# Optimization experiments

Measured on AMD Instinct MI355X. Metric: run time of the kernel, lower is better.

## Reference

```python
import jax, jax.numpy as jnp
import numpy as np

N = 100000   # nodes
M = 200000   # gathered (combined-subgraph) node entries
E = 600000   # combined-subgraph edges
B = 128      # graphs
P = 32       # patches per graph (METIS)
BP = B * P
DIN = 64; H = 256; RW = 16
L = 4        # GCN layers
LM = 4       # mixer layers
T = 64       # token-mixing hidden dim
CH = 4 * H   # channel-mixing hidden dim
DOUT = 10


def _seg_mean(v, idx, n):
    s = jax.ops.segment_sum(v, idx, num_segments=n)
    c = jax.ops.segment_sum(jnp.ones((v.shape[0],), v.dtype), idx, num_segments=n)
    return s / jnp.maximum(c, 1.0)[:, None]


def _ln(x, s, b):
    m = jnp.mean(x, -1, keepdims=True)
    v = jnp.var(x, -1, keepdims=True)
    return (x - m) * jax.lax.rsqrt(v + 1e-5) * s + b


def setup_inputs() -> dict:
    key = jax.random.key(0)
    ks = jax.random.split(key, 40)
    w = lambda k, s: jax.random.normal(k, s, jnp.float32) * 0.02
    inp = {
        'x': jax.random.normal(ks[0], (N, DIN), jnp.float32),
        'patch_pe': jax.random.normal(ks[1], (BP, RW), jnp.float32),
        'mask': jnp.ones((B, P), jnp.bool_),
        'nodes_mapper': jax.random.randint(ks[2], (M,), 0, N),
        'subgraphs_batch': jnp.sort(jax.random.randint(ks[3], (M,), 0, BP)),
        'edge_index': jax.random.randint(ks[4], (2, E), 0, M),
        # pre_mp
        'W_pre': w(ks[5], (DIN, H)), 'b_pre': jnp.zeros((H,), jnp.float32),
        # U MLPs (layers-1 of them) and GCN weights
        'W_u': w(ks[6], (L - 1, H, H)), 'b_u': jnp.zeros((L - 1, H), jnp.float32),
        'W_g': w(ks[7], (L, H, H)), 'b_g': jnp.zeros((L, H), jnp.float32),
        # patch RW-PE 2-layer MLP
        'Wp1': w(ks[8], (RW, H)), 'bp1': jnp.zeros((H,), jnp.float32),
        'Wp2': w(ks[9], (H, H)), 'bp2': jnp.zeros((H,), jnp.float32),
        # MLPMixer blocks (stacked over LM layers)
        'ln1_s': jnp.ones((LM, H), jnp.float32), 'ln1_b': jnp.zeros((LM, H), jnp.float32),
        'Wt1': w(ks[10], (LM, P, T)), 'bt1': jnp.zeros((LM, T), jnp.float32),
        'Wt2': w(ks[11], (LM, T, P)), 'bt2': jnp.zeros((LM, P), jnp.float32),
        'ln2_s': jnp.ones((LM, H), jnp.float32), 'ln2_b': jnp.zeros((LM, H), jnp.float32),
        'Wc1': w(ks[12], (LM, H, CH)), 'bc1': jnp.zeros((LM, CH), jnp.float32),
        'Wc2': w(ks[13], (LM, CH, H)), 'bc2': jnp.zeros((LM, H), jnp.float32),
        # head
        'ln_f_s': jnp.ones((H,), jnp.float32), 'ln_f_b': jnp.zeros((H,), jnp.float32),
        'W_head': w(ks[14], (H, DOUT)), 'b_head': jnp.zeros((DOUT,), jnp.float32),
    }
    return inp


def reference(x, patch_pe, mask, nodes_mapper, subgraphs_batch, edge_index,
              W_pre, b_pre, W_u, b_u, W_g, b_g, Wp1, bp1, Wp2, bp2,
              ln1_s, ln1_b, Wt1, bt1, Wt2, bt2, ln2_s, ln2_b, Wc1, bc1, Wc2, bc2,
              ln_f_s, ln_f_b, W_head, b_head):
    # pre_mp: linear + relu on node features [N, H]
    h = jax.nn.relu(x @ W_pre + b_pre)
    # gather nodes into combined-subgraph space [M, H]
    h = h[nodes_mapper]
    src, dst = edge_index[0], edge_index[1]
    # GCN symmetric normalization with self loops (degree over M-space)
    deg = jax.ops.segment_sum(jnp.ones((src.shape[0],), h.dtype), dst, num_segments=M) + 1.0
    nrm = jax.lax.rsqrt(deg)
    edge_nrm = (nrm[src] * nrm[dst])[:, None]
    self_nrm = (nrm * nrm)[:, None]
    for i in range(L):
        if i > 0:
            # pre_layer_scatter: pool per subgraph, broadcast back, add U-MLP
            sub = _seg_mean(h, subgraphs_batch, BP)[subgraphs_batch]
            h = h + jax.nn.relu(sub @ W_u[i - 1] + b_u[i - 1])
            # post_layer_scatter: mean over duplicated nodes, broadcast back
            h = _seg_mean(h, nodes_mapper, N)[nodes_mapper]
        # GCNConv + relu
        hw = h @ W_g[i]
        agg = jax.ops.segment_sum(hw[src] * edge_nrm, dst, num_segments=M)
        h = jax.nn.relu(agg + hw * self_nrm + b_g[i])
    # final_scatter: pool to [B*P, H]
    h = _seg_mean(h, subgraphs_batch, BP)
    # patch random-walk PE encoder (2-layer MLP) added
    pe = jax.nn.relu(jax.nn.relu(patch_pe @ Wp1 + bp1) @ Wp2 + bp2)
    z = (h + pe).reshape(B, P, H)
    # MLPMixer
    for l in range(LM):
        y = jnp.swapaxes(_ln(z, ln1_s[l], ln1_b[l]), 1, 2)  # [B, H, P]
        y = jax.nn.gelu(y @ Wt1[l] + bt1[l]) @ Wt2[l] + bt2[l]
        z = z + jnp.swapaxes(y, 1, 2)
        y = _ln(z, ln2_s[l], ln2_b[l])
        z = z + (jax.nn.gelu(y @ Wc1[l] + bc1[l]) @ Wc2[l] + bc2[l])
    # masked mean pooling over patches
    m = mask.astype(z.dtype)
    g = (z * m[:, :, None]).sum(1) / m.sum(1, keepdims=True)
    # head
    g = _ln(g, ln_f_s, ln_f_b)
    return g @ W_head + b_head
```

## Files before the change

kernel.cpp:

```cpp
#include <hip/hip_runtime.h>
#include <math.h>

namespace {

typedef unsigned short u16;
typedef unsigned int u32;
typedef unsigned long long u64;
typedef __attribute__((ext_vector_type(8))) short bf16x8;
typedef __attribute__((ext_vector_type(8))) unsigned short u16x8;
typedef __attribute__((ext_vector_type(4))) float f32x4;

constexpr int kN = 100000, kM = 200000, kE = 600000;
constexpr int kB = 128, kP = 32, kBP = kB * kP;
constexpr int kDIN = 64, kH = 256, kRW = 16;
constexpr int kL = 4, kLM = 4, kT = 64, kCH = 4 * kH, kDOUT = 10;
constexpr int kScanCB = 1024;

__device__ __forceinline__ float geluf(float x) {
  const float c = 0.7978845608028654f;
  float x3 = x * x * x;
  return 0.5f * x * (1.f + tanhf(c * (x + 0.044715f * x3)));
}

__device__ __forceinline__ float bf2f(u16 h) {
  u32 u = ((u32)h) << 16;
  return __uint_as_float(u);
}
__device__ __forceinline__ u16 f2bf(float f) {
  u32 u = __float_as_uint(f);
  u32 r = (u + 0x7FFFu + ((u >> 16) & 1u)) >> 16;
  return (u16)r;
}
__device__ __forceinline__ float4 bf4_to_f4(ushort4 v) {
  return make_float4(bf2f(v.x), bf2f(v.y), bf2f(v.z), bf2f(v.w));
}
__device__ __forceinline__ ushort4 f4_to_bf4(float4 v) {
  ushort4 r;
  r.x = f2bf(v.x); r.y = f2bf(v.y); r.z = f2bf(v.z); r.w = f2bf(v.w);
  return r;
}

template <int RPT>
__global__ __launch_bounds__(256) void k_gemm(
    const float* __restrict__ A, const float* __restrict__ B,
    const float* __restrict__ bias, const float* __restrict__ res,
    float* __restrict__ C, int Mr, int Nc, int Kc, int act) {
  constexpr int BM = 16 * RPT;
  __shared__ float As[16][BM];
  __shared__ float Bs[16][64];
  int tid = threadIdx.x;
  int tx = tid & 15, ty = tid >> 4;
  int bm = blockIdx.x * BM, bn = blockIdx.y * 64;
  float acc[RPT][4];
#pragma unroll
  for (int i = 0; i < RPT; ++i)
#pragma unroll
    for (int j = 0; j < 4; ++j) acc[i][j] = 0.f;

  for (int k0 = 0; k0 < Kc; k0 += 16) {
#pragma unroll
    for (int l = 0; l < RPT / 4; ++l) {
      int idx = tid + l * 256;
      int r = idx >> 2, c4 = (idx & 3) * 4;
      float4 a4 = make_float4(0.f, 0.f, 0.f, 0.f);
      if (bm + r < Mr) a4 = *(const float4*)(A + (size_t)(bm + r) * Kc + k0 + c4);
      As[c4 + 0][r] = a4.x; As[c4 + 1][r] = a4.y;
      As[c4 + 2][r] = a4.z; As[c4 + 3][r] = a4.w;
    }
    {
      int kr = tid >> 4, cc = (tid & 15) * 4;
      float4 b4 = *(const float4*)(B + (size_t)(k0 + kr) * Nc + bn + cc);
      *(float4*)&Bs[kr][cc] = b4;
    }
    __syncthreads();
#pragma unroll
    for (int k = 0; k < 16; ++k) {
      float a[RPT], bb[4];
#pragma unroll
      for (int l = 0; l < RPT / 4; ++l) {
        float4 av = *(const float4*)&As[k][ty * RPT + l * 4];
        a[l * 4 + 0] = av.x; a[l * 4 + 1] = av.y;
        a[l * 4 + 2] = av.z; a[l * 4 + 3] = av.w;
      }
      float4 bv = *(const float4*)&Bs[k][tx * 4];
      bb[0] = bv.x; bb[1] = bv.y; bb[2] = bv.z; bb[3] = bv.w;
#pragma unroll
      for (int i = 0; i < RPT; ++i)
#pragma unroll
        for (int j = 0; j < 4; ++j) acc[i][j] = fmaf(a[i], bb[j], acc[i][j]);
    }
    __syncthreads();
  }
#pragma unroll
  for (int i = 0; i < RPT; ++i) {
    int row = bm + ty * RPT + i;
    if (row >= Mr) continue;
#pragma unroll
    for (int j = 0; j < 4; ++j) {
      int col = bn + tx * 4 + j;
      float v = acc[i][j];
      if (bias) v += bias[col];
      if (act == 1) v = fmaxf(v, 0.f);
      else if (act == 2) v = geluf(v);
      if (res) v += res[(size_t)row * Nc + col];
      C[(size_t)row * Nc + col] = v;
    }
  }
}

__global__ void k_packw(const float* __restrict__ W, u16* __restrict__ Wp,
                        int KB, int NC, int L) {
  int per = KB * NC * 16 * 64;
  int o8 = blockIdx.x * 256 + threadIdx.x;
  if (o8 >= L * per) return;
  int li = o8 / per, r = o8 % per;
  int l = r & 63;
  int t = r >> 6;
  int nt = t & 15, q = t >> 4;
  int kbg = q % KB, nc = q / KB;
  int Kc = KB * 32, Ncols = NC * 256;
  int col = nc * 256 + nt * 16 + (l & 15);
  int k0 = kbg * 32 + (l >> 4) * 8;
  const float* w = W + (size_t)li * Kc * Ncols;
  u16* o = Wp + (size_t)o8 * 8;
#pragma unroll
  for (int i = 0; i < 8; ++i) o[i] = f2bf(w[(size_t)(k0 + i) * Ncols + col]);
}

__global__ __launch_bounds__(256) void k_gemm_rowblk_mfma(
    const u16* A, const u16* __restrict__ Wp, u16* C, int Mr) {
  __shared__ u16 As[64 * 256];
  __shared__ u16 Bs[8192];
  int tid = threadIdx.x;
  int w = tid >> 6, l = tid & 63;
  int bm = blockIdx.x * 64;
  u16x8 pre[4];
#pragma unroll
  for (int j = 0; j < 4; ++j) pre[j] = *(const u16x8*)(Wp + tid * 8 + j * 2048);
#pragma unroll
  for (int i = 0; i < 8; ++i) {
    int idx = tid + i * 256;
    int row = idx >> 5, seg = idx & 31;
    u16x8 v = (u16x8){0, 0, 0, 0, 0, 0, 0, 0};
    if (bm + row < Mr) v = *(const u16x8*)(A + (size_t)(bm + row) * 256 + seg * 8);
    *(u16x8*)((char*)As + row * 512 + ((seg * 16) ^ ((row & 15) << 4))) = v;
  }

  f32x4 acc[16];
#pragma unroll
  for (int nt = 0; nt < 16; ++nt) acc[nt] = (f32x4){0.f, 0.f, 0.f, 0.f};
  int a_row = w * 16 + (l & 15);
  int a_xor = (a_row & 15) << 4;
  for (int kb = 0; kb < 8; ++kb) {
    __syncthreads();
#pragma unroll
    for (int j = 0; j < 4; ++j) *(u16x8*)(Bs + tid * 8 + j * 2048) = pre[j];
    __syncthreads();
    if (kb < 7) {
#pragma unroll
      for (int j = 0; j < 4; ++j)
        pre[j] = *(const u16x8*)(Wp + (kb + 1) * 8192 + tid * 8 + j * 2048);
    }
    int abyte = a_row * 512 + ((kb * 64 + (l >> 4) * 16) ^ a_xor);
    bf16x8 af = *(const bf16x8*)((const char*)As + abyte);
#pragma unroll
    for (int nt = 0; nt < 16; ++nt) {
      bf16x8 bf = *(const bf16x8*)(Bs + nt * 512 + l * 8);
      acc[nt] = __builtin_amdgcn_mfma_f32_16x16x32_bf16(af, bf, acc[nt], 0, 0, 0);
    }
  }
  __syncthreads();
  int c_row0 = w * 16 + (l >> 4) * 4;
  int ccol = l & 15;
#pragma unroll
  for (int nt = 0; nt < 16; ++nt) {
#pragma unroll
    for (int j = 0; j < 4; ++j) {
      int row = c_row0 + j;
      int colbyte = (nt * 16 + ccol) * 2;
      *(u16*)((char*)As + row * 512 + (colbyte ^ ((row & 15) << 4))) = f2bf(acc[nt][j]);
    }
  }
  __syncthreads();
#pragma unroll
  for (int i = 0; i < 8; ++i) {
    int idx = tid + i * 256;
    int row = idx >> 5, seg = idx & 31;
    if (bm + row < Mr) {
      u16x8 v = *(const u16x8*)((const char*)As + row * 512 + ((seg * 16) ^ ((row & 15) << 4)));
      *(u16x8*)(C + (size_t)(bm + row) * 256 + seg * 8) = v;
    }
  }
}

__global__ __launch_bounds__(256) void k_gemm_mfma_s(
    const void* __restrict__ Av, const u16* __restrict__ Wp,
    const float* __restrict__ bias, const float* __restrict__ res,
    void* __restrict__ Cv, int Kc, int Ncols, int act, int outw, int abf) {
  __shared__ u16 As[64 * 256];
  __shared__ u16 Bs[8192];
  int tid = threadIdx.x;
  int w = tid >> 6, l = tid & 63;
  int bm = blockIdx.x * 64;
  int nchunk = blockIdx.y, bn = nchunk * 256;
  int KB = Kc >> 5;
  const u16* wseq = Wp + (size_t)nchunk * KB * 8192;

  u16x8 pre[4];
#pragma unroll
  for (int j = 0; j < 4; ++j) pre[j] = *(const u16x8*)(wseq + tid * 8 + j * 2048);

  f32x4 acc[16];
#pragma unroll
  for (int nt = 0; nt < 16; ++nt) acc[nt] = (f32x4){0.f, 0.f, 0.f, 0.f};
  int a_row = w * 16 + (l & 15);
  int a_xor = (a_row & 15) << 4;

  for (int kc0 = 0; kc0 < Kc; kc0 += 256) {
    __syncthreads();
#pragma unroll
    for (int i = 0; i < 8; ++i) {
      int idx = tid + i * 256;
      int row = idx >> 5, seg = idx & 31;
      u16x8 hv;
      if (abf) {
        hv = *(const u16x8*)((const u16*)Av + (size_t)(bm + row) * Kc + kc0 + seg * 8);
      } else {
        const float* s = (const float*)Av + (size_t)(bm + row) * Kc + kc0 + seg * 8;
        float4 v0 = *(const float4*)s;
        float4 v1 = *(const float4*)(s + 4);
        hv[0] = f2bf(v0.x); hv[1] = f2bf(v0.y); hv[2] = f2bf(v0.z); hv[3] = f2bf(v0.w);
        hv[4] = f2bf(v1.x); hv[5] = f2bf(v1.y); hv[6] = f2bf(v1.z); hv[7] = f2bf(v1.w);
      }
      *(u16x8*)((char*)As + row * 512 + ((seg * 16) ^ ((row & 15) << 4))) = hv;
    }
    int kbg0 = kc0 >> 5;
    for (int kb = 0; kb < 8; ++kb) {
      int t = kbg0 + kb;
      __syncthreads();
#pragma unroll
      for (int j = 0; j < 4; ++j) *(u16x8*)(Bs + tid * 8 + j * 2048) = pre[j];
      __syncthreads();
      if (t + 1 < KB) {
#pragma unroll
        for (int j = 0; j < 4; ++j)
          pre[j] = *(const u16x8*)(wseq + (size_t)(t + 1) * 8192 + tid * 8 + j * 2048);
      }
      int abyte = a_row * 512 + ((kb * 64 + (l >> 4) * 16) ^ a_xor);
      bf16x8 af = *(const bf16x8*)((const char*)As + abyte);
#pragma unroll
      for (int nt = 0; nt < 16; ++nt) {
        bf16x8 bf = *(const bf16x8*)(Bs + nt * 512 + l * 8);
        acc[nt] = __builtin_amdgcn_mfma_f32_16x16x32_bf16(af, bf, acc[nt], 0, 0, 0);
      }
    }
  }

  int c_row0 = w * 16 + (l >> 4) * 4;
  int ccol = l & 15;
  if (outw == 1) {
    float* C = (float*)Cv;
#pragma unroll
    for (int nt = 0; nt < 16; ++nt) {
      int col = bn + nt * 16 + ccol;
      float bv = bias[col];
#pragma unroll
      for (int j = 0; j < 4; ++j) {
        int row = bm + c_row0 + j;
        float v = acc[nt][j] + bv;
        if (act == 1) v = fmaxf(v, 0.f);
        else if (act == 2) v = geluf(v);
        if (res) v += res[(size_t)row * Ncols + col];
        C[(size_t)row * Ncols + col] = v;
      }
    }
  } else {
    u16* C = (u16*)Cv;
    __syncthreads();
#pragma unroll
    for (int nt = 0; nt < 16; ++nt) {
      float bv = bias[bn + nt * 16 + ccol];
#pragma unroll
      for (int j = 0; j < 4; ++j) {
        int row = c_row0 + j;
        float v = acc[nt][j] + bv;
        if (act == 1) v = fmaxf(v, 0.f);
        else if (act == 2) v = geluf(v);
        int colbyte = (nt * 16 + ccol) * 2;
        *(u16*)((char*)As + row * 512 + (colbyte ^ ((row & 15) << 4))) = f2bf(v);
      }
    }
    __syncthreads();
#pragma unroll
    for (int i = 0; i < 8; ++i) {
      int idx = tid + i * 256;
      int row = idx >> 5, seg = idx & 31;
      u16x8 v = *(const u16x8*)((const char*)As + row * 512 + ((seg * 16) ^ ((row & 15) << 4)));
      *(u16x8*)(C + (size_t)(bm + row) * Ncols + bn + seg * 8) = v;
    }
  }
}

__global__ __launch_bounds__(256) void k_premp_mfma(
    const float* __restrict__ A, const u16* __restrict__ Wp,
    const float* __restrict__ bias, u16* __restrict__ C, int Mr) {
  __shared__ u16 As[64 * 256];
  __shared__ u16 Bs[8192];
  int tid = threadIdx.x;
  int w = tid >> 6, l = tid & 63;
  int bm = blockIdx.x * 64;
  u16x8 pre[4];
#pragma unroll
  for (int j = 0; j < 4; ++j) pre[j] = *(const u16x8*)(Wp + tid * 8 + j * 2048);
#pragma unroll
  for (int i = 0; i < 2; ++i) {
    int idx = tid + i * 256;
    int row = idx >> 3, seg = idx & 7;
    u16x8 hv = (u16x8){0, 0, 0, 0, 0, 0, 0, 0};
    if (bm + row < Mr) {
      const float* s = A + (size_t)(bm + row) * 64 + seg * 8;
      float4 v0 = *(const float4*)s;
      float4 v1 = *(const float4*)(s + 4);
      hv[0] = f2bf(v0.x); hv[1] = f2bf(v0.y); hv[2] = f2bf(v0.z); hv[3] = f2bf(v0.w);
      hv[4] = f2bf(v1.x); hv[5] = f2bf(v1.y); hv[6] = f2bf(v1.z); hv[7] = f2bf(v1.w);
    }
    *(u16x8*)((char*)As + row * 128 + ((seg * 16) ^ ((row & 7) << 4))) = hv;
  }

  f32x4 acc[16];
#pragma unroll
  for (int nt = 0; nt < 16; ++nt) acc[nt] = (f32x4){0.f, 0.f, 0.f, 0.f};
  int a_row = w * 16 + (l & 15);
#pragma unroll
  for (int kb = 0; kb < 2; ++kb) {
    __syncthreads();
#pragma unroll
    for (int j = 0; j < 4; ++j) *(u16x8*)(Bs + tid * 8 + j * 2048) = pre[j];
    __syncthreads();
    if (kb == 0) {
#pragma unroll
      for (int j = 0; j < 4; ++j)
        pre[j] = *(const u16x8*)(Wp + 8192 + tid * 8 + j * 2048);
    }
    int abyte = a_row * 128 + ((kb * 64 + (l >> 4) * 16) ^ ((a_row & 7) << 4));
    bf16x8 af = *(const bf16x8*)((const char*)As + abyte);
#pragma unroll
    for (int nt = 0; nt < 16; ++nt) {
      bf16x8 bf = *(const bf16x8*)(Bs + nt * 512 + l * 8);
      acc[nt] = __builtin_amdgcn_mfma_f32_16x16x32_bf16(af, bf, acc[nt], 0, 0, 0);
    }
  }
  __syncthreads();
  int c_row0 = w * 16 + (l >> 4) * 4;
  int ccol = l & 15;
#pragma unroll
  for (int nt = 0; nt < 16; ++nt) {
    float bv = bias[nt * 16 + ccol];
#pragma unroll
    for (int j = 0; j < 4; ++j) {
      int row = c_row0 + j;
      float v = fmaxf(acc[nt][j] + bv, 0.f);
      int colbyte = (nt * 16 + ccol) * 2;
      *(u16*)((char*)As + row * 512 + (colbyte ^ ((row & 15) << 4))) = f2bf(v);
    }
  }
  __syncthreads();
#pragma unroll
  for (int i = 0; i < 8; ++i) {
    int idx = tid + i * 256;
    int row = idx >> 5, seg = idx & 31;
    if (bm + row < Mr) {
      u16x8 v = *(const u16x8*)((const char*)As + row * 512 + ((seg * 16) ^ ((row & 15) << 4)));
      *(u16x8*)(C + (size_t)(bm + row) * 256 + seg * 8) = v;
    }
  }
}

__global__ void k_hist(const int* __restrict__ idx, int* __restrict__ cnt, int n) {
  int i = blockIdx.x * 256 + threadIdx.x;
  if (i < n) atomicAdd(&cnt[idx[i]], 1);
}

__global__ __launch_bounds__(256) void k_scan_a(const int* __restrict__ cnt, int n,
                                                int* __restrict__ bsum) {
  __shared__ int red[256];
  int b = blockIdx.x, t = threadIdx.x;
  int base = b * kScanCB + t * 4;
  int s = 0;
#pragma unroll
  for (int j = 0; j < 4; ++j) { int i = base + j; if (i < n) s += cnt[i]; }
  red[t] = s;
  __syncthreads();
  for (int d = 128; d; d >>= 1) {
    if (t < d) red[t] += red[t + d];
    __syncthreads();
  }
  if (t == 0) bsum[b] = red[0];
}

__global__ __launch_bounds__(256) void k_scan_b(const int* __restrict__ bsum, int G,
                                                int* __restrict__ boff,
                                                int* __restrict__ total_out) {
  __shared__ int sd[256];
  int t = threadIdx.x;
  sd[t] = (t < G) ? bsum[t] : 0;
  __syncthreads();
  for (int d = 1; d < 256; d <<= 1) {
    int u = (t >= d) ? sd[t - d] : 0;
    __syncthreads();
    sd[t] += u;
    __syncthreads();
  }
  if (t < G) boff[t] = t ? sd[t - 1] : 0;
  if (t == 255) *total_out = sd[255];
}

__global__ __launch_bounds__(256) void k_scan_c(const int* __restrict__ cnt, int n,
                                                const int* __restrict__ boff,
                                                int* __restrict__ out) {
  __shared__ int sd[256];
  int b = blockIdx.x, t = threadIdx.x;
  int base = b * kScanCB + t * 4;
  int c[4];
  int s = 0;
#pragma unroll
  for (int j = 0; j < 4; ++j) {
    int i = base + j;
    c[j] = (i < n) ? cnt[i] : 0;
    s += c[j];
  }
  sd[t] = s;
  __syncthreads();
  for (int d = 1; d < 256; d <<= 1) {
    int u = (t >= d) ? sd[t - d] : 0;
    __syncthreads();
    sd[t] += u;
    __syncthreads();
  }
  int run = boff[b] + (t ? sd[t - 1] : 0);
#pragma unroll
  for (int j = 0; j < 4; ++j) {
    int i = base + j;
    if (i < n) out[i] = run;
    run += c[j];
  }
}

__global__ void k_nrm(const int* __restrict__ cnt, float* __restrict__ nrm, int n) {
  int i = blockIdx.x * 256 + threadIdx.x;
  if (i < n) nrm[i] = rsqrtf((float)cnt[i] + 1.f);
}

__global__ void k_scatter_e(const int* __restrict__ src, const int* __restrict__ dst,
                            const int* __restrict__ nmap, const float* __restrict__ nrm,
                            const int* __restrict__ rs, int* __restrict__ cur,
                            int* __restrict__ gidx, float* __restrict__ w) {
  int e = blockIdx.x * 256 + threadIdx.x;
  if (e >= kE) return;
  int s = src[e], d = dst[e];
  int p = rs[d] + atomicAdd(&cur[d], 1);
  gidx[p] = nmap[s];
  w[p] = nrm[s] * nrm[d];
}

__global__ void k_scatter_m(const int* __restrict__ nmap, const int* __restrict__ rs,
                            int* __restrict__ cur, int* __restrict__ lst) {
  int m = blockIdx.x * 256 + threadIdx.x;
  if (m >= kM) return;
  int n = nmap[m];
  int p = rs[n] + atomicAdd(&cur[n], 1);
  lst[p] = m;
}

__global__ void k_bpstart(const int* __restrict__ sb, int* __restrict__ bps) {
  int bp = blockIdx.x * 256 + threadIdx.x;
  if (bp > kBP) return;
  if (bp == kBP) { bps[kBP] = kM; return; }
  int lo = 0, hi = kM;
  while (lo < hi) { int mid = (lo + hi) >> 1; if (sb[mid] < bp) lo = mid + 1; else hi = mid; }
  bps[bp] = lo;
}

__global__ __launch_bounds__(256) void k_pool_seg_b(const u16* __restrict__ h,
                                                    const int* __restrict__ bps,
                                                    float* __restrict__ out) {
  int bp = blockIdx.x, j = threadIdx.x;
  int lo = bps[bp], hi = bps[bp + 1];
  float s = 0.f;
  for (int m = lo; m < hi; ++m) s += bf2f(h[(size_t)m * kH + j]);
  out[(size_t)bp * kH + j] = s / fmaxf((float)(hi - lo), 1.f);
}

__global__ __launch_bounds__(256) void k_pool_n_f(const u16* __restrict__ h,
                                                  const float* __restrict__ ub,
                                                  const int* __restrict__ sb,
                                                  const int* __restrict__ rs,
                                                  const int* __restrict__ lst,
                                                  u16* __restrict__ outp) {
  int wv = threadIdx.x >> 6, lane = threadIdx.x & 63;
  int n = blockIdx.x * 4 + wv;
  if (n >= kN) return;
  int lo = rs[n], hi = rs[n + 1];
  float4 acc = make_float4(0.f, 0.f, 0.f, 0.f);
  for (int p = lo; p < hi; ++p) {
    int m = lst[p];
    union { u64 u; ushort4 s; } cv;
    cv.u = __builtin_nontemporal_load((const u64*)(h + (size_t)m * 256 + lane * 4));
    float4 v = bf4_to_f4(cv.s);
    float4 u = ((const float4*)ub)[(size_t)sb[m] * 64 + lane];
    acc.x += v.x + u.x; acc.y += v.y + u.y;
    acc.z += v.z + u.z; acc.w += v.w + u.w;
  }
  float inv = 1.f / fmaxf((float)(hi - lo), 1.f);
  acc.x *= inv; acc.y *= inv; acc.z *= inv; acc.w *= inv;
  *(ushort4*)(outp + (size_t)n * 256 + lane * 4) = f4_to_bf4(acc);
}

__global__ __launch_bounds__(256) void k_gcn_b(const u16* __restrict__ hw,
                                               const int* __restrict__ nmap,
                                               const float* __restrict__ nrm,
                                               const int* __restrict__ rs,
                                               const int* __restrict__ gidx,
                                               const float* __restrict__ w,
                                               const float* __restrict__ bias,
                                               u16* __restrict__ outp) {
  int wv = threadIdx.x >> 6, lane = threadIdx.x & 63;
  int m = blockIdx.x * 4 + wv;
  if (m >= kM) return;
  float nm_ = nrm[m];
  float sn = nm_ * nm_;
  float4 b4 = ((const float4*)bias)[lane];
  float4 sv = bf4_to_f4(*(const ushort4*)(hw + (size_t)nmap[m] * 256 + lane * 4));
  float4 acc;
  acc.x = fmaf(sv.x, sn, b4.x); acc.y = fmaf(sv.y, sn, b4.y);
  acc.z = fmaf(sv.z, sn, b4.z); acc.w = fmaf(sv.w, sn, b4.w);
  int lo = rs[m], hi = rs[m + 1];
  for (int p0 = lo; p0 < hi; p0 += 4) {
    int last = hi - 1;
    int q1 = min(p0 + 1, last), q2 = min(p0 + 2, last), q3 = min(p0 + 3, last);
    int g0 = gidx[p0], g1 = gidx[q1], g2 = gidx[q2], g3 = gidx[q3];
    float w0 = w[p0];
    float w1 = (p0 + 1 < hi) ? w[q1] : 0.f;
    float w2 = (p0 + 2 < hi) ? w[q2] : 0.f;
    float w3 = (p0 + 3 < hi) ? w[q3] : 0.f;
    float4 v0 = bf4_to_f4(*(const ushort4*)(hw + (size_t)g0 * 256 + lane * 4));
    float4 v1 = bf4_to_f4(*(const ushort4*)(hw + (size_t)g1 * 256 + lane * 4));
    float4 v2 = bf4_to_f4(*(const ushort4*)(hw + (size_t)g2 * 256 + lane * 4));
    float4 v3 = bf4_to_f4(*(const ushort4*)(hw + (size_t)g3 * 256 + lane * 4));
    acc.x = fmaf(v3.x, w3, fmaf(v2.x, w2, fmaf(v1.x, w1, fmaf(v0.x, w0, acc.x))));
    acc.y = fmaf(v3.y, w3, fmaf(v2.y, w2, fmaf(v1.y, w1, fmaf(v0.y, w0, acc.y))));
    acc.z = fmaf(v3.z, w3, fmaf(v2.z, w2, fmaf(v1.z, w1, fmaf(v0.z, w0, acc.z))));
    acc.w = fmaf(v3.w, w3, fmaf(v2.w, w2, fmaf(v1.w, w1, fmaf(v0.w, w0, acc.w))));
  }
  acc.x = fmaxf(acc.x, 0.f); acc.y = fmaxf(acc.y, 0.f);
  acc.z = fmaxf(acc.z, 0.f); acc.w = fmaxf(acc.w, 0.f);
  *(ushort4*)(outp + (size_t)m * 256 + lane * 4) = f4_to_bf4(acc);
}

__global__ __launch_bounds__(256) void k_ln(const float* __restrict__ x,
                                            const float* __restrict__ s,
                                            const float* __restrict__ b,
                                            float* __restrict__ y) {
  __shared__ float t1[4], t2[4];
  int r = blockIdx.x, j = threadIdx.x;
  float v = x[(size_t)r * kH + j];
  float a = v, q = v * v;
  for (int o = 32; o; o >>= 1) { a += __shfl_down(a, o, 64); q += __shfl_down(q, o, 64); }
  if ((j & 63) == 0) { t1[j >> 6] = a; t2[j >> 6] = q; }
  __syncthreads();
  float sum = t1[0] + t1[1] + t1[2] + t1[3];
  float sq = t2[0] + t2[1] + t2[2] + t2[3];
  float mu = sum * (1.f / 256.f);
  float var = sq * (1.f / 256.f) - mu * mu;
  y[(size_t)r * kH + j] = (v - mu) * rsqrtf(var + 1e-5f) * s[j] + b[j];
}

__global__ __launch_bounds__(256) void k_token(const float* __restrict__ zn,
                                               const float* __restrict__ Wt1,
                                               const float* __restrict__ bt1,
                                               const float* __restrict__ Wt2,
                                               const float* __restrict__ bt2,
                                               float* __restrict__ z) {
  __shared__ float zs[32][65];
  __shared__ float w1[32][64];
  __shared__ float w2[64][33];
  __shared__ float y1[64][65];
  int bb = blockIdx.x, hb = blockIdx.y * 64;
  int t = threadIdx.x;
  for (int i = t; i < 2048; i += 256) {
    int p = i >> 6, hh = i & 63;
    zs[p][hh] = zn[((size_t)bb * 32 + p) * kH + hb + hh];
  }
  for (int i = t; i < 2048; i += 256) { int p = i >> 6, tt = i & 63; w1[p][tt] = Wt1[p * 64 + tt]; }
  for (int i = t; i < 2048; i += 256) { int tt = i >> 5, p = i & 31; w2[tt][p] = Wt2[tt * 32 + p]; }
  __syncthreads();
  for (int i = t; i < 4096; i += 256) {
    int hh = i >> 6, tt = i & 63;
    float a = bt1[tt];
#pragma unroll
    for (int p = 0; p < 32; ++p) a = fmaf(zs[p][hh], w1[p][tt], a);
    y1[hh][tt] = geluf(a);
  }
  __syncthreads();
  for (int i = t; i < 2048; i += 256) {
    int hh = i >> 5, p = i & 31;
    float a = bt2[p];
#pragma unroll
    for (int tt = 0; tt < 64; ++tt) a = fmaf(y1[hh][tt], w2[tt][p], a);
    z[((size_t)bb * 32 + p) * kH + hb + hh] += a;
  }
}

__global__ void k_gpool(const float* __restrict__ z, float* __restrict__ g) {
  int bb = blockIdx.x, j = threadIdx.x;
  float s = 0.f;
  for (int p = 0; p < 32; ++p) s += z[((size_t)bb * 32 + p) * kH + j];
  g[bb * kH + j] = s * (1.f / 32.f);
}

__global__ __launch_bounds__(256) void k_head(const float* __restrict__ g,
                                              const float* __restrict__ s,
                                              const float* __restrict__ b,
                                              const float* __restrict__ Wh,
                                              const float* __restrict__ bh,
                                              float* __restrict__ out) {
  __shared__ float t1[4], t2[4];
  __shared__ float row[256];
  int bb = blockIdx.x, j = threadIdx.x;
  float v = g[bb * kH + j];
  float a = v, q = v * v;
  for (int o = 32; o; o >>= 1) { a += __shfl_down(a, o, 64); q += __shfl_down(q, o, 64); }
  if ((j & 63) == 0) { t1[j >> 6] = a; t2[j >> 6] = q; }
  __syncthreads();
  float sum = t1[0] + t1[1] + t1[2] + t1[3];
  float sq = t2[0] + t2[1] + t2[2] + t2[3];
  float mu = sum * (1.f / 256.f);
  float var = sq * (1.f / 256.f) - mu * mu;
  row[j] = (v - mu) * rsqrtf(var + 1e-5f) * s[j] + b[j];
  __syncthreads();
  if (j < kDOUT) {
    float acc = bh[j];
    for (int k = 0; k < kH; ++k) acc = fmaf(row[k], Wh[k * kDOUT + j], acc);
    out[bb * kDOUT + j] = acc;
  }
}

}

extern "C" void kernel_launch(void* const* d_in, const int* in_sizes, int n_in,
                              void* d_out, int out_size, void* d_ws, size_t ws_size,
                              hipStream_t stream) {
  const float* x = (const float*)d_in[0];
  const float* ppe = (const float*)d_in[1];
  const int* nmap = (const int*)d_in[3];
  const int* sb = (const int*)d_in[4];
  const int* esrc = (const int*)d_in[5];
  const int* edst = esrc + kE;
  const float* Wpre = (const float*)d_in[6];
  const float* bpre = (const float*)d_in[7];
  const float* Wu = (const float*)d_in[8];
  const float* bu = (const float*)d_in[9];
  const float* Wg = (const float*)d_in[10];
  const float* bg = (const float*)d_in[11];
  const float* Wp1 = (const float*)d_in[12];
  const float* bp1 = (const float*)d_in[13];
  const float* Wp2 = (const float*)d_in[14];
  const float* bp2 = (const float*)d_in[15];
  const float* ln1s = (const float*)d_in[16];
  const float* ln1b = (const float*)d_in[17];
  const float* Wt1 = (const float*)d_in[18];
  const float* bt1 = (const float*)d_in[19];
  const float* Wt2 = (const float*)d_in[20];
  const float* bt2 = (const float*)d_in[21];
  const float* ln2s = (const float*)d_in[22];
  const float* ln2b = (const float*)d_in[23];
  const float* Wc1 = (const float*)d_in[24];
  const float* bc1 = (const float*)d_in[25];
  const float* Wc2 = (const float*)d_in[26];
  const float* bc2 = (const float*)d_in[27];
  const float* lnfs = (const float*)d_in[28];
  const float* lnfb = (const float*)d_in[29];
  const float* Whd = (const float*)d_in[30];
  const float* bhd = (const float*)d_in[31];
  float* out = (float*)d_out;

  u16* h_M = (u16*)d_ws;
  u16* h_N = h_M + (size_t)kM * kH;
  float* sub = (float*)(h_N + (size_t)kN * kH);
  float* ubuf = sub + (size_t)kBP * kH;
  float* csrw = ubuf + (size_t)kBP * kH;
  float* nrm = csrw + kE;
  int* rsE = (int*)(nrm + kM);
  int* gidx = rsE + kM + 1;
  int* rsN = gidx + kE;
  int* mlst = rsN + kN + 1;
  int* cntE = mlst + kM;
  int* cntN = cntE + kM;
  int* bps = cntN + kN;
  int* bsumS = bps + kBP + 1;
  int* boffS = bsumS + 256;
  size_t need = ((size_t)(boffS + 256)) - ((size_t)d_ws);
  if (ws_size < need) {
    hipMemsetAsync(d_out, 0, (size_t)out_size * sizeof(float), stream);
    return;
  }

  u16* wpackG = (u16*)(((size_t)cntE + 15) & ~(size_t)15);
  u16* wpackPre = wpackG + 4 * 65536;
  u16* wpackU = wpackPre + 16384;

  float* z = (float*)d_ws;
  float* zn = z + (size_t)kBP * kH;
  float* c1 = zn + (size_t)kBP * kH;
  float* g = c1 + (size_t)kBP * kCH;
  u16* wpackC = (u16*)(g + kB * kH);
  u16* wpackC2 = wpackC + 4 * 262144;
  u16* wpackP2 = wpackC2 + 4 * 262144;

  hipMemsetAsync(cntE, 0, kM * sizeof(int), stream);
  hipMemsetAsync(cntN, 0, kN * sizeof(int), stream);

  constexpr int GscanM = (kM + kScanCB - 1) / kScanCB;
  constexpr int GscanN = (kN + kScanCB - 1) / kScanCB;

  k_hist<<<(kE + 255) / 256, 256, 0, stream>>>(edst, cntE, kE);
  k_hist<<<(kM + 255) / 256, 256, 0, stream>>>(nmap, cntN, kM);
  k_scan_a<<<GscanM, 256, 0, stream>>>(cntE, kM, bsumS);
  k_scan_b<<<1, 256, 0, stream>>>(bsumS, GscanM, boffS, rsE + kM);
  k_scan_c<<<GscanM, 256, 0, stream>>>(cntE, kM, boffS, rsE);
  k_scan_a<<<GscanN, 256, 0, stream>>>(cntN, kN, bsumS);
  k_scan_b<<<1, 256, 0, stream>>>(bsumS, GscanN, boffS, rsN + kN);
  k_scan_c<<<GscanN, 256, 0, stream>>>(cntN, kN, boffS, rsN);
  k_nrm<<<(kM + 255) / 256, 256, 0, stream>>>(cntE, nrm, kM);
  hipMemsetAsync(cntE, 0, kM * sizeof(int), stream);
  hipMemsetAsync(cntN, 0, kN * sizeof(int), stream);
  k_scatter_e<<<(kE + 255) / 256, 256, 0, stream>>>(esrc, edst, nmap, nrm, rsE, cntE, gidx, csrw);
  k_scatter_m<<<(kM + 255) / 256, 256, 0, stream>>>(nmap, rsN, cntN, mlst);
  k_bpstart<<<(kBP + 256) / 256, 256, 0, stream>>>(sb, bps);
  k_packw<<<(4 * 8192 + 255) / 256, 256, 0, stream>>>(Wg, wpackG, 8, 1, 4);
  k_packw<<<(2048 + 255) / 256, 256, 0, stream>>>(Wpre, wpackPre, 2, 1, 1);
  k_packw<<<(3 * 8192 + 255) / 256, 256, 0, stream>>>(Wu, wpackU, 8, 1, 3);

  k_premp_mfma<<<(kN + 63) / 64, 256, 0, stream>>>(x, wpackPre, bpre, h_N, kN);

  for (int i = 0; i < kL; ++i) {
    if (i > 0) {
      k_pool_seg_b<<<kBP, 256, 0, stream>>>(h_M, bps, sub);
      k_gemm_mfma_s<<<dim3(64, 1), 256, 0, stream>>>(
          sub, wpackU + (size_t)(i - 1) * 65536, bu + (i - 1) * kH, nullptr,
          ubuf, 256, 256, 1, 1, 0);
      k_pool_n_f<<<(kN + 3) / 4, 256, 0, stream>>>(h_M, ubuf, sb, rsN, mlst, h_N);
    }
    k_gemm_rowblk_mfma<<<(kN + 63) / 64, 256, 0, stream>>>(
        h_N, wpackG + (size_t)i * 65536, h_N, kN);
    k_gcn_b<<<(kM + 3) / 4, 256, 0, stream>>>(h_N, nmap, nrm, rsE, gidx, csrw, bg + i * kH, h_M);
  }

  k_pool_seg_b<<<kBP, 256, 0, stream>>>(h_M, bps, sub);
  k_packw<<<(4 * 32768 + 255) / 256, 256, 0, stream>>>(Wc1, wpackC, 8, 4, 4);
  k_packw<<<(4 * 32768 + 255) / 256, 256, 0, stream>>>(Wc2, wpackC2, 32, 1, 4);
  k_packw<<<(8192 + 255) / 256, 256, 0, stream>>>(Wp2, wpackP2, 8, 1, 1);

  dim3 gBP4((kBP + 63) / 64, kH / 64);
  k_gemm<4><<<gBP4, 256, 0, stream>>>(ppe, Wp1, bp1, nullptr, ubuf, kBP, kH, kRW, 1);
  k_gemm_mfma_s<<<dim3(64, 1), 256, 0, stream>>>(ubuf, wpackP2, bp2, sub, z, 256, 256, 1, 1, 0);

  for (int l = 0; l < kLM; ++l) {
    k_ln<<<kBP, 256, 0, stream>>>(z, ln1s + l * kH, ln1b + l * kH, zn);
    dim3 gt(kB, kH / 64);
    k_token<<<gt, 256, 0, stream>>>(zn, Wt1 + l * kP * kT, bt1 + l * kT,
                                    Wt2 + l * kT * kP, bt2 + l * kP, z);
    k_ln<<<kBP, 256, 0, stream>>>(z, ln2s + l * kH, ln2b + l * kH, zn);
    k_gemm_mfma_s<<<dim3(64, 4), 256, 0, stream>>>(
        zn, wpackC + (size_t)l * 262144, bc1 + l * kCH, nullptr,
        (u16*)c1, 256, 1024, 2, 0, 0);
    k_gemm_mfma_s<<<dim3(64, 1), 256, 0, stream>>>(
        (const u16*)c1, wpackC2 + (size_t)l * 262144, bc2 + l * kH, z,
        z, 1024, 256, 0, 1, 1);
  }

  k_gpool<<<kB, 256, 0, stream>>>(z, g);
  k_head<<<kB, 256, 0, stream>>>(g, lnfs, lnfb, Whd, bhd, out);
}
```

Measured before the change: 1.406 ms.

## Split-K the channel-mix down-projection with atomics and widen pooling kernels' parallelism

The Wc2 GEMM (K=1024) now runs split-K over four z-slices, each block accumulating its partial into z with float atomicAdd, and the bias is added only by the first slice. Before, that GEMM ran on only 64 blocks. The residual is now implicit because z is accumulated in place. The patch-mean pooling now spreads rows across four waves with vectorised bf16x4 loads and a shared-memory reduction, and the node-pool loop is unrolled by two to issue more independent loads. In exchange, atomics make the summation order nondeterministic and add atomic traffic on z.

After: 1.206 ms. 14.2% less time.

```diff
diff --git a/kernel.cpp b/kernel.cpp
--- a/kernel.cpp
+++ b/kernel.cpp
@@ -196,19 +196,21 @@
 __global__ __launch_bounds__(256) void k_gemm_mfma_s(
     const void* __restrict__ Av, const u16* __restrict__ Wp,
     const float* __restrict__ bias, const float* __restrict__ res,
-    void* __restrict__ Cv, int Kc, int Ncols, int act, int outw, int abf) {
+    void* __restrict__ Cv, int Kc, int Ncols, int act, int outw, int abf, int kclen) {
   __shared__ u16 As[64 * 256];
   __shared__ u16 Bs[8192];
   int tid = threadIdx.x;
   int w = tid >> 6, l = tid & 63;
   int bm = blockIdx.x * 64;
   int nchunk = blockIdx.y, bn = nchunk * 256;
+  int kcs = blockIdx.z * kclen;
   int KB = Kc >> 5;
   const u16* wseq = Wp + (size_t)nchunk * KB * 8192;
 
   u16x8 pre[4];
 #pragma unroll
-  for (int j = 0; j < 4; ++j) pre[j] = *(const u16x8*)(wseq + tid * 8 + j * 2048);
+  for (int j = 0; j < 4; ++j)
+    pre[j] = *(const u16x8*)(wseq + (size_t)(kcs >> 5) * 8192 + tid * 8 + j * 2048);
 
   f32x4 acc[16];
 #pragma unroll
@@ -216,7 +218,7 @@
   int a_row = w * 16 + (l & 15);
   int a_xor = (a_row & 15) << 4;
 
-  for (int kc0 = 0; kc0 < Kc; kc0 += 256) {
+  for (int kc0 = kcs; kc0 < kcs + kclen; kc0 += 256) {
     __syncthreads();
 #pragma unroll
     for (int i = 0; i < 8; ++i) {
@@ -258,7 +260,20 @@
 
   int c_row0 = w * 16 + (l >> 4) * 4;
   int ccol = l & 15;
-  if (outw == 1) {
+  if (outw == 2) {
+    float* C = (float*)Cv;
+    bool addb = (kcs == 0);
+#pragma unroll
+    for (int nt = 0; nt < 16; ++nt) {
+      int col = bn + nt * 16 + ccol;
+      float bv = addb ? bias[col] : 0.f;
+#pragma unroll
+      for (int j = 0; j < 4; ++j) {
+        int row = bm + c_row0 + j;
+        atomicAdd(&C[(size_t)row * Ncols + col], acc[nt][j] + bv);
+      }
+    }
+  } else if (outw == 1) {
     float* C = (float*)Cv;
 #pragma unroll
     for (int nt = 0; nt < 16; ++nt) {
@@ -484,11 +499,20 @@
 __global__ __launch_bounds__(256) void k_pool_seg_b(const u16* __restrict__ h,
                                                     const int* __restrict__ bps,
                                                     float* __restrict__ out) {
-  int bp = blockIdx.x, j = threadIdx.x;
+  __shared__ float red[4][256];
+  int bp = blockIdx.x;
+  int tid = threadIdx.x;
+  int wv = tid >> 6, lane = tid & 63;
   int lo = bps[bp], hi = bps[bp + 1];
-  float s = 0.f;
-  for (int m = lo; m < hi; ++m) s += bf2f(h[(size_t)m * kH + j]);
-  out[(size_t)bp * kH + j] = s / fmaxf((float)(hi - lo), 1.f);
+  float4 acc = make_float4(0.f, 0.f, 0.f, 0.f);
+  for (int m = lo + wv; m < hi; m += 4) {
+    float4 v = bf4_to_f4(*(const ushort4*)(h + (size_t)m * 256 + lane * 4));
+    acc.x += v.x; acc.y += v.y; acc.z += v.z; acc.w += v.w;
+  }
+  *(float4*)&red[wv][lane * 4] = acc;
+  __syncthreads();
+  float s = red[0][tid] + red[1][tid] + red[2][tid] + red[3][tid];
+  out[(size_t)bp * kH + tid] = s / fmaxf((float)(hi - lo), 1.f);
 }
 
 __global__ __launch_bounds__(256) void k_pool_n_f(const u16* __restrict__ h,
@@ -502,14 +526,18 @@
   if (n >= kN) return;
   int lo = rs[n], hi = rs[n + 1];
   float4 acc = make_float4(0.f, 0.f, 0.f, 0.f);
-  for (int p = lo; p < hi; ++p) {
-    int m = lst[p];
-    union { u64 u; ushort4 s; } cv;
-    cv.u = __builtin_nontemporal_load((const u64*)(h + (size_t)m * 256 + lane * 4));
-    float4 v = bf4_to_f4(cv.s);
-    float4 u = ((const float4*)ub)[(size_t)sb[m] * 64 + lane];
-    acc.x += v.x + u.x; acc.y += v.y + u.y;
-    acc.z += v.z + u.z; acc.w += v.w + u.w;
+  for (int p = lo; p < hi; p += 2) {
+    int p1 = min(p + 1, hi - 1);
+    int m0 = lst[p], m1 = lst[p1];
+    float c1 = (p + 1 < hi) ? 1.f : 0.f;
+    float4 v0 = bf4_to_f4(*(const ushort4*)(h + (size_t)m0 * 256 + lane * 4));
+    float4 v1 = bf4_to_f4(*(const ushort4*)(h + (size_t)m1 * 256 + lane * 4));
+    float4 u0 = ((const float4*)ub)[(size_t)sb[m0] * 64 + lane];
+    float4 u1 = ((const float4*)ub)[(size_t)sb[m1] * 64 + lane];
+    acc.x += v0.x + u0.x + c1 * (v1.x + u1.x);
+    acc.y += v0.y + u0.y + c1 * (v1.y + u1.y);
+    acc.z += v0.z + u0.z + c1 * (v1.z + u1.z);
+    acc.w += v0.w + u0.w + c1 * (v1.w + u1.w);
   }
   float inv = 1.f / fmaxf((float)(hi - lo), 1.f);
   acc.x *= inv; acc.y *= inv; acc.z *= inv; acc.w *= inv;
@@ -748,7 +776,7 @@
       k_pool_seg_b<<<kBP, 256, 0, stream>>>(h_M, bps, sub);
       k_gemm_mfma_s<<<dim3(64, 1), 256, 0, stream>>>(
           sub, wpackU + (size_t)(i - 1) * 65536, bu + (i - 1) * kH, nullptr,
-          ubuf, 256, 256, 1, 1, 0);
+          ubuf, 256, 256, 1, 1, 0, 256);
       k_pool_n_f<<<(kN + 3) / 4, 256, 0, stream>>>(h_M, ubuf, sb, rsN, mlst, h_N);
     }
     k_gemm_rowblk_mfma<<<(kN + 63) / 64, 256, 0, stream>>>(
@@ -763,7 +791,8 @@
 
   dim3 gBP4((kBP + 63) / 64, kH / 64);
   k_gemm<4><<<gBP4, 256, 0, stream>>>(ppe, Wp1, bp1, nullptr, ubuf, kBP, kH, kRW, 1);
-  k_gemm_mfma_s<<<dim3(64, 1), 256, 0, stream>>>(ubuf, wpackP2, bp2, sub, z, 256, 256, 1, 1, 0);
+  k_gemm_mfma_s<<<dim3(64, 1), 256, 0, stream>>>(ubuf, wpackP2, bp2, sub, z,
+                                                 256, 256, 1, 1, 0, 256);
 
   for (int l = 0; l < kLM; ++l) {
     k_ln<<<kBP, 256, 0, stream>>>(z, ln1s + l * kH, ln1b + l * kH, zn);
@@ -773,10 +802,10 @@
     k_ln<<<kBP, 256, 0, stream>>>(z, ln2s + l * kH, ln2b + l * kH, zn);
     k_gemm_mfma_s<<<dim3(64, 4), 256, 0, stream>>>(
         zn, wpackC + (size_t)l * 262144, bc1 + l * kCH, nullptr,
-        (u16*)c1, 256, 1024, 2, 0, 0);
-    k_gemm_mfma_s<<<dim3(64, 1), 256, 0, stream>>>(
-        (const u16*)c1, wpackC2 + (size_t)l * 262144, bc2 + l * kH, z,
-        z, 1024, 256, 0, 1, 1);
+        (u16*)c1, 256, 1024, 2, 0, 0, 256);
+    k_gemm_mfma_s<<<dim3(64, 1, 4), 256, 0, stream>>>(
+        (const u16*)c1, wpackC2 + (size_t)l * 262144, bc2 + l * kH, nullptr,
+        z, 1024, 256, 0, 2, 1, 256);
   }
 
   k_gpool<<<kB, 256, 0, stream>>>(z, g);
```
